# Performance work log

Measured on AMD Instinct MI355X. Metric: run time of the kernel, lower is better.

The kernel has to match this reference:

```python
import jax, jax.numpy as jnp
import numpy as np

B, S, D_IN, D_MID, D_OUT, V = 32, 512, 768, 128, 4, 100000
N = B * S  # static upper bound on number of unique (vocab_id, batch_id) pairs


def setup_inputs() -> dict:
    key = jax.random.key(0)
    k1, k2, k3, k4 = jax.random.split(key, 4)
    vocab_ids = jax.random.randint(k1, (B, S), 0, V)
    embeddings = jax.random.normal(k2, (B, S, D_IN), jnp.float32)
    # nn.Linear default init (kaiming-uniform-ish); exact distribution is irrelevant for correctness
    lin_bound = 1.0 / np.sqrt(D_IN)
    W1 = jax.random.uniform(k3, (D_IN, D_MID), jnp.float32, -lin_bound, lin_bound)
    b1 = jnp.zeros((D_MID,), jnp.float32)
    # kaiming_uniform_(a=sqrt(5)) on (V, D_MID, D_OUT): fan_in = D_MID*D_OUT, bound = 1/sqrt(fan_in)
    enc_bound = 1.0 / np.sqrt(D_MID * D_OUT)
    encoder_weights = jax.random.uniform(k4, (V, D_MID, D_OUT), jnp.float32, -enc_bound, enc_bound)
    return {"vocab_ids": vocab_ids, "embeddings": embeddings, "W1": W1, "b1": b1,
            "encoder_weights": encoder_weights}


def reference(vocab_ids, embeddings, W1, b1, encoder_weights):
    # Composite key = vocab_id * B + batch_id -> same lexicographic (vocab, batch) order
    # as torch.unique(dim=0) on stacked (vocab_id, batch_id) pairs.
    batch_ids = jnp.arange(B, dtype=vocab_ids.dtype)[:, None]            # (B,1)
    keys = (vocab_ids * B + batch_ids).reshape(-1)                        # (N,)
    # Static-size unique for jit; padded slots (fill) receive zero-sum embeddings.
    uniq_keys, inv = jnp.unique(keys, size=N, fill_value=0, return_inverse=True)
    flat_emb = embeddings.reshape(N, D_IN)
    summed = jax.ops.segment_sum(flat_emb, inv.reshape(-1), num_segments=N)  # (N, D_IN)
    h = jnp.tanh(summed @ W1 + b1)                                        # (N, D_MID)
    uniq_vocab = uniq_keys // B
    uniq_batch = uniq_keys % B
    Wtok = encoder_weights[uniq_vocab]                                    # (N, D_MID, D_OUT) gather
    encoded = jax.nn.sigmoid(jnp.einsum('bi,bio->bo', h, Wtok))           # (N, D_OUT)
    ids = jnp.stack([uniq_vocab, uniq_batch], axis=1)                     # (N, 2)
    return ids, encoded
```

## Files before the change

kernel.cpp:

```cpp
#include <hip/hip_runtime.h>
#include <hip/hip_bf16.h>

#define NELEM 16384
#define DIN 768
#define DMID 128
#define DOUT 4
#define NBWPAD 114688
#define BMBYTES 458752

typedef __attribute__((ext_vector_type(8))) short short8;
typedef __attribute__((ext_vector_type(4))) float f32x4;

__device__ __forceinline__ unsigned f2bf(float f) {
    unsigned u = __float_as_uint(f);
    return (u + 0x7FFFu + ((u >> 16) & 1u)) >> 16;
}
__device__ __forceinline__ void aor(unsigned* p, unsigned v) {
    __hip_atomic_fetch_or(p, v, __ATOMIC_RELAXED, __HIP_MEMORY_SCOPE_AGENT);
}
__device__ __forceinline__ unsigned wscan_inc(unsigned x, int lane) {
    unsigned inc = x;
#pragma unroll
    for (int off = 1; off < 64; off <<= 1) {
        unsigned y = __shfl_up(inc, off);
        if (lane >= off) inc += y;
    }
    return inc;
}
__device__ __forceinline__ unsigned popc4(uint4 x) {
    return (unsigned)(__popc(x.x) + __popc(x.y) + __popc(x.z) + __popc(x.w));
}

#define FAST4_WS 917632

__global__ __launch_bounds__(256) void prep_kernel(
    const int* __restrict__ vocab_ids, const float* __restrict__ W1,
    unsigned* __restrict__ Gb, unsigned short* __restrict__ WtG,
    unsigned* __restrict__ bitmap, unsigned long long* __restrict__ stage,
    unsigned* __restrict__ LCnt) {
    __shared__ unsigned lbm[4096];
    __shared__ unsigned voc[512];
    __shared__ unsigned short gel[512];
    __shared__ unsigned gcnt[512];
    __shared__ unsigned gstart[512];
    __shared__ unsigned part[256];
    __shared__ unsigned wsumL[4];

    const int t = threadIdx.x;
    const int b = blockIdx.x;
    const int lane = t & 63;
    const int wv = t >> 6;

#pragma unroll
    for (int i = 0; i < 12; ++i) {
        int j = b * 3072 + i * 256 + t;
        int k = j >> 7, c = j & 127;
        WtG[c * DIN + k] = (unsigned short)f2bf(W1[j]);
    }

#pragma unroll
    for (int i = 0; i < 16; ++i) lbm[t + 256 * i] = 0;
    gcnt[t] = 0; gcnt[t + 256] = 0;
#pragma unroll
    for (int q = 0; q < 2; ++q) {
        int s = q * 256 + t;
        unsigned v = (unsigned)vocab_ids[b * 512 + s];
        voc[s] = v;
        unsigned key = v * 32u + (unsigned)b;
        aor(&bitmap[key >> 5], 1u << (key & 31u));
    }
    __syncthreads();
#pragma unroll
    for (int q = 0; q < 2; ++q) {
        unsigned v = voc[q * 256 + t];
        atomicOr(&lbm[v >> 5], 1u << (v & 31u));
    }
    __syncthreads();
    {
        unsigned sum = 0;
#pragma unroll
        for (int j = 0; j < 16; ++j) sum += (unsigned)__popc(lbm[t * 16 + j]);
        unsigned inc = wscan_inc(sum, lane);
        if (lane == 63) wsumL[wv] = inc;
        __syncthreads();
        unsigned woff = 0;
        for (int i = 0; i < wv; ++i) woff += wsumL[i];
        part[t] = woff + inc - sum;
        if (t == 255) LCnt[b] = woff + inc;
        __syncthreads();
    }
#pragma unroll
    for (int q = 0; q < 2; ++q) {
        int s = q * 256 + t;
        unsigned v = voc[s];
        unsigned lw = v >> 5, c = lw >> 4;
        unsigned g = part[c];
        for (unsigned j = c * 16; j < lw; ++j) g += (unsigned)__popc(lbm[j]);
        g += (unsigned)__popc(lbm[lw] & ((1u << (v & 31u)) - 1u));
        gel[s] = (unsigned short)g;
        atomicAdd(&gcnt[g], 1u);
    }
    __syncthreads();
    {
        unsigned a = gcnt[2 * t], b2 = gcnt[2 * t + 1];
        unsigned pair = a + b2;
        unsigned inc = wscan_inc(pair, lane);
        if (lane == 63) wsumL[wv] = inc;
        __syncthreads();
        unsigned woff = 0;
        for (int i = 0; i < wv; ++i) woff += wsumL[i];
        unsigned excl = woff + inc - pair;
        gstart[2 * t] = excl;
        gstart[2 * t + 1] = excl + a;
    }
    __syncthreads();
#pragma unroll
    for (int q = 0; q < 2; ++q) {
        int s = q * 256 + t;
        unsigned g = gel[s];
        unsigned v = voc[s];
        unsigned m = 0;
        if (gcnt[g] > 1) {
            for (int j = 0; j < s; ++j) if (voc[j] == v) ++m;
        }
        Gb[b * 512 + gstart[g] + m] = (v << 9) | (unsigned)s;
        if (m == 0) {
            unsigned sdval = ((unsigned)b << 19) | (gstart[g] << 10) | gcnt[g];
            stage[b * 512 + g] = ((unsigned long long)v << 32) | sdval;
        }
    }
}

__global__ __launch_bounds__(256) void rank_kernel(
    const unsigned* __restrict__ bitmap,
    const unsigned long long* __restrict__ stage,
    const unsigned* __restrict__ LCnt,
    unsigned* __restrict__ SD, float* __restrict__ out_ids) {
    __shared__ unsigned pre16[7168];
    __shared__ unsigned wsumL[4];
    __shared__ unsigned Ush;

    const int t = threadIdx.x;
    const int b = blockIdx.x;
    const int lane = t & 63;
    const int wv = t >> 6;
    const uint4* bm4 = (const uint4*)bitmap;

    unsigned locpre[28];
    unsigned run = 0;
    {
        const uint4* my = bm4 + t * 112;
#pragma unroll
        for (int g = 0; g < 28; ++g) {
            locpre[g] = run;
#pragma unroll
            for (int q = 0; q < 4; ++q) run += popc4(my[g * 4 + q]);
        }
        unsigned inc = wscan_inc(run, lane);
        if (lane == 63) wsumL[wv] = inc;
        __syncthreads();
        unsigned woff = 0;
        for (int i = 0; i < wv; ++i) woff += wsumL[i];
        unsigned excl = woff + inc - run;
#pragma unroll
        for (int g = 0; g < 28; ++g) pre16[t * 28 + g] = excl + locpre[g];
        if (t == 255) Ush = woff + inc;
        __syncthreads();
    }
    const unsigned U = Ush;

    const unsigned cnt = LCnt[b];
    for (unsigned l = t; l < cnt; l += 256) {
        unsigned long long sv = stage[b * 512 + l];
        unsigned v = (unsigned)(sv >> 32);
        unsigned sdval = (unsigned)sv;
        unsigned key = v * 32u + (unsigned)b;
        unsigned w = key >> 5, bit = key & 31u;
        unsigned rank = pre16[w >> 4];
        const uint4* gp = bm4 + ((w >> 4) << 2);
        unsigned wq = (w >> 2) & 3u;
        for (unsigned q = 0; q < wq; ++q) rank += popc4(gp[q]);
        uint4 x = gp[wq];
        unsigned ww = w & 3u;
        if (ww > 0) rank += (unsigned)__popc(x.x);
        if (ww > 1) rank += (unsigned)__popc(x.y);
        if (ww > 2) rank += (unsigned)__popc(x.z);
        unsigned wword = (ww == 0) ? x.x : (ww == 1) ? x.y : (ww == 2) ? x.z : x.w;
        rank += (unsigned)__popc(wword & ((1u << bit) - 1u));
        SD[rank] = sdval;
        out_ids[2 * rank + 0] = (float)v;
        out_ids[2 * rank + 1] = (float)((sdval >> 19) & 31u);
    }
    for (int u = (int)U + b * 256 + t; u < NELEM; u += 32 * 256) {
        SD[u] = 0u;
        out_ids[2 * u + 0] = 0.0f;
        out_ids[2 * u + 1] = 0.0f;
    }
}

#define FBM 16
__global__ __launch_bounds__(256) void fused_kernel(
    const unsigned* __restrict__ Gb,
    const unsigned* __restrict__ SD,
    const unsigned short* __restrict__ WtG,
    const float* __restrict__ emb,
    const float* __restrict__ b1,
    const float* __restrict__ enc,
    float* __restrict__ out_enc) {
    __shared__ char smem[20736];

    const int t = threadIdx.x;
    const int u0 = blockIdx.x * FBM;
    const int l = t & 63;
    const int w = t >> 6;

    const int ar = t >> 4;
    const int ak4 = t & 15;
    const unsigned sdw = SD[u0 + ar];
    const int lenA = (int)(sdw & 1023u);
    const unsigned embBase = (sdw >> 19) << 9;
    const unsigned gb0 = embBase + ((sdw >> 10) & 511u);

    f32x4 acc0 = {0.f, 0.f, 0.f, 0.f};
    f32x4 acc1 = {0.f, 0.f, 0.f, 0.f};

    for (int kk = 0; kk < DIN; kk += 64) {
        __syncthreads();
        {
            float s0 = 0.f, s1 = 0.f, s2 = 0.f, s3 = 0.f;
            const float* base = emb + (size_t)(kk + ak4 * 4);
            for (int p = 0; p < lenA; ++p) {
                unsigned idx = embBase + (Gb[gb0 + p] & 511u);
                const float4 e4 = *(const float4*)(base + (size_t)idx * DIN);
                s0 += e4.x; s1 += e4.y; s2 += e4.z; s3 += e4.w;
            }
            uint2 packed;
            packed.x = f2bf(s0) | (f2bf(s1) << 16);
            packed.y = f2bf(s2) | (f2bf(s3) << 16);
            *(uint2*)(smem + ar * 144 + ak4 * 8) = packed;
        }
        {
#pragma unroll
            for (int i = 0; i < 4; ++i) {
                int q = t + i * 256;
                int c = q >> 3;
                int uo = q & 7;
                uint4 dv = *(const uint4*)(WtG + (size_t)c * DIN + kk + uo * 8);
                *(uint4*)(smem + 2304 + c * 144 + uo * 16) = dv;
            }
        }
        __syncthreads();
        {
            const int arow = l & 15;
            const int ull = l >> 4;
#pragma unroll
            for (int kf = 0; kf < 2; ++kf) {
                short8 aF = *(const short8*)(smem + arow * 144 + kf * 64 + ull * 16);
                short8 bF0 = *(const short8*)(smem + 2304 + (w * 32 + arow) * 144 + kf * 64 + ull * 16);
                short8 bF1 = *(const short8*)(smem + 2304 + (w * 32 + 16 + arow) * 144 + kf * 64 + ull * 16);
                acc0 = __builtin_amdgcn_mfma_f32_16x16x32_bf16(aF, bF0, acc0, 0, 0, 0);
                acc1 = __builtin_amdgcn_mfma_f32_16x16x32_bf16(aF, bF1, acc1, 0, 0, 0);
            }
        }
    }
    __syncthreads();
    {
        float* Hs = (float*)smem;
        const int col0 = w * 32 + (l & 15);
        const int rbase = (l >> 4) * 4;
#pragma unroll
        for (int reg = 0; reg < 4; ++reg) {
            Hs[(rbase + reg) * 132 + col0] = tanhf(acc0[reg] + b1[col0]);
            Hs[(rbase + reg) * 132 + col0 + 16] = tanhf(acc1[reg] + b1[col0 + 16]);
        }
    }
    __syncthreads();
    {
        const float* Hs = (const float*)smem;
        const int r = t >> 4;
        const int g = t & 15;
        const int u = u0 + r;
        const unsigned sdw2 = SD[u];
        unsigned vocab = 0;
        if (sdw2 & 1023u)
            vocab = Gb[((sdw2 >> 19) << 9) + ((sdw2 >> 10) & 511u)] >> 9;
        const float4* wrow = (const float4*)(enc + (size_t)vocab * (DMID * DOUT));
        float ax = 0.f, ay = 0.f, az = 0.f, aw = 0.f;
#pragma unroll
        for (int jj = 0; jj < 8; ++jj) {
            int j = jj * 16 + g;
            float4 w4 = wrow[j];
            float hv = Hs[r * 132 + j];
            ax += hv * w4.x; ay += hv * w4.y; az += hv * w4.z; aw += hv * w4.w;
        }
#pragma unroll
        for (int off = 1; off < 16; off <<= 1) {
            ax += __shfl_xor(ax, off);
            ay += __shfl_xor(ay, off);
            az += __shfl_xor(az, off);
            aw += __shfl_xor(aw, off);
        }
        if (g == 0) {
            float4 o;
            o.x = 1.f / (1.f + expf(-ax));
            o.y = 1.f / (1.f + expf(-ay));
            o.z = 1.f / (1.f + expf(-az));
            o.w = 1.f / (1.f + expf(-aw));
            *(float4*)(out_enc + (size_t)u * 4) = o;
        }
    }
}

#define SORT_SMEM (65536 + 65536 + 4096 + 64)

__global__ __launch_bounds__(1024) void sort_transpose_kernel(
    const int* __restrict__ vocab_ids,
    const float* __restrict__ W1,
    unsigned int* __restrict__ G,
    unsigned short* __restrict__ RS,
    unsigned short* __restrict__ WtG,
    float* __restrict__ out_ids) {
    const int t = threadIdx.x;
    if (blockIdx.x != 0) {
        int idx = (blockIdx.x - 1) * 1024 + t;
        if (idx < DMID * DIN) {
            int c = idx / DIN;
            int k = idx - c * DIN;
            WtG[idx] = (unsigned short)f2bf(W1[k * DMID + c]);
        }
        return;
    }
    extern __shared__ char smem[];
    unsigned* Gs     = (unsigned*)smem;
    unsigned* histDM = (unsigned*)(smem + 65536);
    unsigned* sums   = (unsigned*)(smem + 131072);
    unsigned* totalU = (unsigned*)(smem + 135168);
    for (int e = t; e < NELEM; e += 1024)
        Gs[e] = ((unsigned)vocab_ids[e] << 14) | (unsigned)e;
    __syncthreads();
    for (int pass = 0; pass < 6; ++pass) {
        const int shift = 9 + pass * 4;
        unsigned v[16];
#pragma unroll
        for (int i = 0; i < 16; ++i) v[i] = Gs[t * 16 + i];
#pragma unroll
        for (int d = 0; d < 16; ++d) histDM[d * 1024 + t] = 0;
#pragma unroll
        for (int i = 0; i < 16; ++i) histDM[((v[i] >> shift) & 15u) * 1024 + t] += 1;
        __syncthreads();
        unsigned lex[16]; unsigned run = 0;
#pragma unroll
        for (int i = 0; i < 16; ++i) { unsigned x = histDM[t * 16 + i]; lex[i] = run; run += x; }
        sums[t] = run;
        __syncthreads();
        if (t < 64) {
            unsigned s[16]; unsigned tot = 0;
#pragma unroll
            for (int i = 0; i < 16; ++i) { unsigned x = sums[t * 16 + i]; s[i] = tot; tot += x; }
            unsigned incv = tot;
#pragma unroll
            for (int off = 1; off < 64; off <<= 1) {
                unsigned y = __shfl_up(incv, off);
                if (t >= off) incv += y;
            }
            unsigned excl = incv - tot;
#pragma unroll
            for (int i = 0; i < 16; ++i) sums[t * 16 + i] = excl + s[i];
        }
        __syncthreads();
#pragma unroll
        for (int i = 0; i < 16; ++i) histDM[t * 16 + i] = sums[t] + lex[i];
        __syncthreads();
        unsigned mycnt[16];
#pragma unroll
        for (int d = 0; d < 16; ++d) mycnt[d] = histDM[d * 1024 + t];
#pragma unroll
        for (int i = 0; i < 16; ++i) {
            unsigned d = (v[i] >> shift) & 15u;
            Gs[mycnt[d]++] = v[i];
        }
        __syncthreads();
    }
    unsigned v[16];
#pragma unroll
    for (int i = 0; i < 16; ++i) v[i] = Gs[t * 16 + i];
    unsigned pk = (t == 0) ? 0xFFFFFFFFu : (Gs[t * 16 - 1] >> 9);
    unsigned fm = 0;
#pragma unroll
    for (int i = 0; i < 16; ++i) {
        unsigned key = v[i] >> 9;
        if (key != pk) fm |= (1u << i);
        pk = key;
    }
    sums[t] = (unsigned)__popc(fm);
    __syncthreads();
    if (t < 64) {
        unsigned s[16]; unsigned tot = 0;
#pragma unroll
        for (int i = 0; i < 16; ++i) { unsigned x = sums[t * 16 + i]; s[i] = tot; tot += x; }
        unsigned incv = tot;
#pragma unroll
        for (int off = 1; off < 64; off <<= 1) {
            unsigned y = __shfl_up(incv, off);
            if (t >= off) incv += y;
        }
        unsigned excl = incv - tot;
#pragma unroll
        for (int i = 0; i < 16; ++i) sums[t * 16 + i] = excl + s[i];
        if (t == 63) *totalU = incv;
    }
    __syncthreads();
    unsigned r = sums[t];
#pragma unroll
    for (int i = 0; i < 16; ++i) {
        if (fm & (1u << i)) {
            RS[r] = (unsigned short)(t * 16 + i);
            out_ids[2 * r + 0] = (float)(v[i] >> 14);
            out_ids[2 * r + 1] = (float)((v[i] >> 9) & 31u);
            ++r;
        }
    }
    const unsigned U = *totalU;
    for (int u = t; u < NELEM; u += 1024) {
        if ((unsigned)u >= U) {
            RS[u] = (unsigned short)NELEM;
            out_ids[2 * u + 0] = 0.0f;
            out_ids[2 * u + 1] = 0.0f;
        }
        G[u] = Gs[u];
    }
    if (t == 0) RS[NELEM] = (unsigned short)NELEM;
}

__global__ __launch_bounds__(256) void fused_kernel_rs(
    const unsigned* __restrict__ G,
    const unsigned short* __restrict__ RS,
    const unsigned short* __restrict__ WtG,
    const float* __restrict__ emb,
    const float* __restrict__ b1,
    const float* __restrict__ enc,
    float* __restrict__ out_enc) {
    __shared__ char smem[20736];
    const int t = threadIdx.x;
    const int u0 = blockIdx.x * FBM;
    const int l = t & 63;
    const int w = t >> 6;
    const int ar = t >> 4;
    const int ak4 = t & 15;
    const int rs_a = (int)RS[u0 + ar];
    const int re_a = (int)RS[u0 + ar + 1];
    f32x4 acc0 = {0.f, 0.f, 0.f, 0.f};
    f32x4 acc1 = {0.f, 0.f, 0.f, 0.f};
    for (int kk = 0; kk < DIN; kk += 64) {
        __syncthreads();
        {
            float s0 = 0.f, s1 = 0.f, s2 = 0.f, s3 = 0.f;
            const float* base = emb + (size_t)(kk + ak4 * 4);
            for (int p = rs_a; p < re_a; ++p) {
                unsigned idx = G[p] & 16383u;
                const float4 e4 = *(const float4*)(base + (size_t)idx * DIN);
                s0 += e4.x; s1 += e4.y; s2 += e4.z; s3 += e4.w;
            }
            uint2 packed;
            packed.x = f2bf(s0) | (f2bf(s1) << 16);
            packed.y = f2bf(s2) | (f2bf(s3) << 16);
            *(uint2*)(smem + ar * 144 + ak4 * 8) = packed;
        }
        {
#pragma unroll
            for (int i = 0; i < 4; ++i) {
                int q = t + i * 256;
                int c = q >> 3;
                int uo = q & 7;
                uint4 dv = *(const uint4*)(WtG + (size_t)c * DIN + kk + uo * 8);
                *(uint4*)(smem + 2304 + c * 144 + uo * 16) = dv;
            }
        }
        __syncthreads();
        {
            const int arow = l & 15;
            const int ull = l >> 4;
#pragma unroll
            for (int kf = 0; kf < 2; ++kf) {
                short8 aF = *(const short8*)(smem + arow * 144 + kf * 64 + ull * 16);
                short8 bF0 = *(const short8*)(smem + 2304 + (w * 32 + arow) * 144 + kf * 64 + ull * 16);
                short8 bF1 = *(const short8*)(smem + 2304 + (w * 32 + 16 + arow) * 144 + kf * 64 + ull * 16);
                acc0 = __builtin_amdgcn_mfma_f32_16x16x32_bf16(aF, bF0, acc0, 0, 0, 0);
                acc1 = __builtin_amdgcn_mfma_f32_16x16x32_bf16(aF, bF1, acc1, 0, 0, 0);
            }
        }
    }
    __syncthreads();
    {
        float* Hs = (float*)smem;
        const int col0 = w * 32 + (l & 15);
        const int rbase = (l >> 4) * 4;
#pragma unroll
        for (int reg = 0; reg < 4; ++reg) {
            Hs[(rbase + reg) * 132 + col0] = tanhf(acc0[reg] + b1[col0]);
            Hs[(rbase + reg) * 132 + col0 + 16] = tanhf(acc1[reg] + b1[col0 + 16]);
        }
    }
    __syncthreads();
    {
        const float* Hs = (const float*)smem;
        const int r = t >> 4;
        const int g = t & 15;
        const int u = u0 + r;
        const int rs = (int)RS[u];
        const int re = (int)RS[u + 1];
        unsigned vocab = (rs < re) ? (G[rs] >> 14) : 0u;
        const float4* wrow = (const float4*)(enc + (size_t)vocab * (DMID * DOUT));
        float ax = 0.f, ay = 0.f, az = 0.f, aw = 0.f;
#pragma unroll
        for (int jj = 0; jj < 8; ++jj) {
            int j = jj * 16 + g;
            float4 w4 = wrow[j];
            float hv = Hs[r * 132 + j];
            ax += hv * w4.x; ay += hv * w4.y; az += hv * w4.z; aw += hv * w4.w;
        }
#pragma unroll
        for (int off = 1; off < 16; off <<= 1) {
            ax += __shfl_xor(ax, off);
            ay += __shfl_xor(ay, off);
            az += __shfl_xor(az, off);
            aw += __shfl_xor(aw, off);
        }
        if (g == 0) {
            float4 o;
            o.x = 1.f / (1.f + expf(-ax));
            o.y = 1.f / (1.f + expf(-ay));
            o.z = 1.f / (1.f + expf(-az));
            o.w = 1.f / (1.f + expf(-aw));
            *(float4*)(out_enc + (size_t)u * 4) = o;
        }
    }
}

extern "C" void kernel_launch(void* const* d_in, const int* in_sizes, int n_in,
                              void* d_out, int out_size, void* d_ws, size_t ws_size,
                              hipStream_t stream) {
    const int*   vocab_ids = (const int*)d_in[0];
    const float* emb       = (const float*)d_in[1];
    const float* W1        = (const float*)d_in[2];
    const float* b1        = (const float*)d_in[3];
    const float* enc       = (const float*)d_in[4];
    float* out = (float*)d_out;
    float* out_ids = out;
    float* out_enc = out + NELEM * 2;
    char* ws = (char*)d_ws;

    if (ws_size >= FAST4_WS) {
        unsigned*           Gb     = (unsigned*)(ws + 0);
        unsigned*           SD     = (unsigned*)(ws + 65536);
        unsigned short*     WtG    = (unsigned short*)(ws + 131072);
        unsigned long long* stage  = (unsigned long long*)(ws + 327680);
        unsigned*           LCnt   = (unsigned*)(ws + 458752);
        unsigned*           bitmap = (unsigned*)(ws + 458880);

        hipMemsetAsync(bitmap, 0, BMBYTES, stream);
        prep_kernel<<<32, 256, 0, stream>>>(vocab_ids, W1, Gb, WtG, bitmap, stage, LCnt);
        rank_kernel<<<32, 256, 0, stream>>>(bitmap, stage, LCnt, SD, out_ids);
        fused_kernel<<<NELEM / FBM, 256, 0, stream>>>(Gb, SD, WtG, emb, b1, enc, out_enc);
    } else {
        unsigned int*   G   = (unsigned int*)(ws);
        unsigned short* RS  = (unsigned short*)(ws + 65536);
        unsigned short* WtG = (unsigned short*)(ws + 98432);

        hipFuncSetAttribute((const void*)sort_transpose_kernel,
                            hipFuncAttributeMaxDynamicSharedMemorySize, SORT_SMEM);
        sort_transpose_kernel<<<1 + 96, 1024, SORT_SMEM, stream>>>(
            vocab_ids, W1, G, RS, WtG, out_ids);
        fused_kernel_rs<<<NELEM / FBM, 256, 0, stream>>>(G, RS, WtG, emb, b1, enc, out_enc);
    }
}
```

Baseline: 69.64 us.

## Replace global atomic key bitmap with per-batch transposed vocab bitmaps

Instead of building a global (vocab*32+batch) bitmap with device-scope atomic ORs after a memset, each prep block writes its local vocab bitmap into a word-major transposed array (word x 32 batches). The rank kernel then builds prefix counts over vocab words and computes each key's rank from the 32 per-batch words of its column, masking bits below and adding lower-batch bits at equal vocab. This drops the memset launch and the global atomics, at the cost of a slightly larger workspace and 32 loads per rank query.

```diff
diff --git a/kernel.cpp b/kernel.cpp
--- a/kernel.cpp
+++ b/kernel.cpp
@@ -5,8 +5,6 @@
 #define DIN 768
 #define DMID 128
 #define DOUT 4
-#define NBWPAD 114688
-#define BMBYTES 458752
 
 typedef __attribute__((ext_vector_type(8))) short short8;
 typedef __attribute__((ext_vector_type(4))) float f32x4;
@@ -15,9 +13,6 @@
     unsigned u = __float_as_uint(f);
     return (u + 0x7FFFu + ((u >> 16) & 1u)) >> 16;
 }
-__device__ __forceinline__ void aor(unsigned* p, unsigned v) {
-    __hip_atomic_fetch_or(p, v, __ATOMIC_RELAXED, __HIP_MEMORY_SCOPE_AGENT);
-}
 __device__ __forceinline__ unsigned wscan_inc(unsigned x, int lane) {
     unsigned inc = x;
 #pragma unroll
@@ -31,12 +26,12 @@
     return (unsigned)(__popc(x.x) + __popc(x.y) + __popc(x.z) + __popc(x.w));
 }
 
-#define FAST4_WS 917632
+#define FAST5_WS 983168
 
 __global__ __launch_bounds__(256) void prep_kernel(
     const int* __restrict__ vocab_ids, const float* __restrict__ W1,
     unsigned* __restrict__ Gb, unsigned short* __restrict__ WtG,
-    unsigned* __restrict__ bitmap, unsigned long long* __restrict__ stage,
+    unsigned* __restrict__ RBT, unsigned long long* __restrict__ stage,
     unsigned* __restrict__ LCnt) {
     __shared__ unsigned lbm[4096];
     __shared__ unsigned voc[512];
@@ -64,10 +59,7 @@
 #pragma unroll
     for (int q = 0; q < 2; ++q) {
         int s = q * 256 + t;
-        unsigned v = (unsigned)vocab_ids[b * 512 + s];
-        voc[s] = v;
-        unsigned key = v * 32u + (unsigned)b;
-        aor(&bitmap[key >> 5], 1u << (key & 31u));
+        voc[s] = (unsigned)vocab_ids[b * 512 + s];
     }
     __syncthreads();
 #pragma unroll
@@ -76,6 +68,11 @@
         atomicOr(&lbm[v >> 5], 1u << (v & 31u));
     }
     __syncthreads();
+#pragma unroll
+    for (int i = 0; i < 16; ++i) {
+        int w = i * 256 + t;
+        RBT[w * 32 + b] = lbm[w];
+    }
     {
         unsigned sum = 0;
 #pragma unroll
@@ -132,11 +129,11 @@
 }
 
 __global__ __launch_bounds__(256) void rank_kernel(
-    const unsigned* __restrict__ bitmap,
+    const unsigned* __restrict__ RBT,
     const unsigned long long* __restrict__ stage,
     const unsigned* __restrict__ LCnt,
     unsigned* __restrict__ SD, float* __restrict__ out_ids) {
-    __shared__ unsigned pre16[7168];
+    __shared__ unsigned pre1[4096];
     __shared__ unsigned wsumL[4];
     __shared__ unsigned Ush;
 
@@ -144,17 +141,19 @@
     const int b = blockIdx.x;
     const int lane = t & 63;
     const int wv = t >> 6;
-    const uint4* bm4 = (const uint4*)bitmap;
-
-    unsigned locpre[28];
-    unsigned run = 0;
-    {
-        const uint4* my = bm4 + t * 112;
-#pragma unroll
-        for (int g = 0; g < 28; ++g) {
-            locpre[g] = run;
-#pragma unroll
-            for (int q = 0; q < 4; ++q) run += popc4(my[g * 4 + q]);
+    const uint4* rb4 = (const uint4*)RBT;
+
+    {
+        unsigned loc[16];
+        unsigned run = 0;
+#pragma unroll
+        for (int i = 0; i < 16; ++i) {
+            loc[i] = run;
+            const uint4* p = rb4 + (t * 16 + i) * 8;
+            unsigned s = 0;
+#pragma unroll
+            for (int q = 0; q < 8; ++q) s += popc4(p[q]);
+            run += s;
         }
         unsigned inc = wscan_inc(run, lane);
         if (lane == 63) wsumL[wv] = inc;
@@ -163,7 +162,7 @@
         for (int i = 0; i < wv; ++i) woff += wsumL[i];
         unsigned excl = woff + inc - run;
 #pragma unroll
-        for (int g = 0; g < 28; ++g) pre16[t * 28 + g] = excl + locpre[g];
+        for (int i = 0; i < 16; ++i) pre1[t * 16 + i] = excl + loc[i];
         if (t == 255) Ush = woff + inc;
         __syncthreads();
     }
@@ -174,22 +173,19 @@
         unsigned long long sv = stage[b * 512 + l];
         unsigned v = (unsigned)(sv >> 32);
         unsigned sdval = (unsigned)sv;
-        unsigned key = v * 32u + (unsigned)b;
-        unsigned w = key >> 5, bit = key & 31u;
-        unsigned rank = pre16[w >> 4];
-        const uint4* gp = bm4 + ((w >> 4) << 2);
-        unsigned wq = (w >> 2) & 3u;
-        for (unsigned q = 0; q < wq; ++q) rank += popc4(gp[q]);
-        uint4 x = gp[wq];
-        unsigned ww = w & 3u;
-        if (ww > 0) rank += (unsigned)__popc(x.x);
-        if (ww > 1) rank += (unsigned)__popc(x.y);
-        if (ww > 2) rank += (unsigned)__popc(x.z);
-        unsigned wword = (ww == 0) ? x.x : (ww == 1) ? x.y : (ww == 2) ? x.z : x.w;
-        rank += (unsigned)__popc(wword & ((1u << bit) - 1u));
+        unsigned w = v >> 5, bit = v & 31u;
+        unsigned maskLT = (1u << bit) - 1u;
+        unsigned rank = pre1[w];
+        const unsigned* col = RBT + w * 32;
+#pragma unroll
+        for (int bb = 0; bb < 32; ++bb) {
+            unsigned word = col[bb];
+            rank += (unsigned)__popc(word & maskLT);
+            if (bb < b) rank += (word >> bit) & 1u;
+        }
         SD[rank] = sdval;
         out_ids[2 * rank + 0] = (float)v;
-        out_ids[2 * rank + 1] = (float)((sdval >> 19) & 31u);
+        out_ids[2 * rank + 1] = (float)b;
     }
     for (int u = (int)U + b * 256 + t; u < NELEM; u += 32 * 256) {
         SD[u] = 0u;
@@ -550,17 +546,16 @@
     float* out_enc = out + NELEM * 2;
     char* ws = (char*)d_ws;
 
-    if (ws_size >= FAST4_WS) {
-        unsigned*           Gb     = (unsigned*)(ws + 0);
-        unsigned*           SD     = (unsigned*)(ws + 65536);
-        unsigned short*     WtG    = (unsigned short*)(ws + 131072);
-        unsigned long long* stage  = (unsigned long long*)(ws + 327680);
-        unsigned*           LCnt   = (unsigned*)(ws + 458752);
-        unsigned*           bitmap = (unsigned*)(ws + 458880);
-
-        hipMemsetAsync(bitmap, 0, BMBYTES, stream);
-        prep_kernel<<<32, 256, 0, stream>>>(vocab_ids, W1, Gb, WtG, bitmap, stage, LCnt);
-        rank_kernel<<<32, 256, 0, stream>>>(bitmap, stage, LCnt, SD, out_ids);
+    if (ws_size >= FAST5_WS) {
+        unsigned*           Gb    = (unsigned*)(ws + 0);
+        unsigned*           SD    = (unsigned*)(ws + 65536);
+        unsigned short*     WtG   = (unsigned short*)(ws + 131072);
+        unsigned long long* stage = (unsigned long long*)(ws + 327680);
+        unsigned*           LCnt  = (unsigned*)(ws + 458752);
+        unsigned*           RBT   = (unsigned*)(ws + 458880);
+
+        prep_kernel<<<32, 256, 0, stream>>>(vocab_ids, W1, Gb, WtG, RBT, stage, LCnt);
+        rank_kernel<<<32, 256, 0, stream>>>(RBT, stage, LCnt, SD, out_ids);
         fused_kernel<<<NELEM / FBM, 256, 0, stream>>>(Gb, SD, WtG, emb, b1, enc, out_enc);
     } else {
         unsigned int*   G   = (unsigned int*)(ws);
```

Measured after the change: 70.07 us. Within noise of the previous version (+0.6%).
